# Performance work log

Hardware: AMD Instinct MI355X
Metric: run time of the kernel (lower is better)

## Reference

```python
import jax, jax.numpy as jnp
import numpy as np
import math

NUM_CLASS = 100000
EMB = 512
N = 1024
S = 64.0
M2 = 0.5
M3 = 0.2
T = 0.2
ERRSUM = 0.3
CLEAR_RIO = 1.0 - ERRSUM
NUM_ALL = 2900.0
GAMMA = 2
EMA = 0.01


def setup_inputs() -> dict:
    key = jax.random.key(0)
    k1, k2, k3 = jax.random.split(key, 3)
    logits = jax.random.normal(k1, (N, EMB), dtype=jnp.float32)
    labels = jax.random.randint(k2, (N,), 0, NUM_CLASS, dtype=jnp.int64)
    weight = jax.random.normal(k3, (NUM_CLASS, EMB), dtype=jnp.float32) * 0.01
    return {"logits": logits, "labels": labels, "weight": weight}


def _l2norm(x):
    return x * jax.lax.rsqrt(jnp.sum(x * x, axis=-1, keepdims=True) + 1e-12)


def reference(logits, labels, weight):
    # margin constants (m_smooth starts at 0, so margin_ada leaves m3 unchanged)
    cos_m, sin_m = math.cos(M2), math.sin(M2)
    theta = math.cos(math.pi - M2)
    sinmm = math.sin(math.pi - M2) * M2
    cos_m_, sin_m_ = math.cos(M3), math.sin(M3)
    sinmm_ = math.sin(-M3) * M3

    # cosine similarity GEMM: [N, C]
    cos = jnp.clip(_l2norm(logits) @ _l2norm(weight).T, -1.0, 1.0)

    rows = jnp.arange(cos.shape[0])
    tgt = cos[rows, labels]                       # [N]
    sin_theta = jnp.sqrt(1.0 - tgt * tgt)
    cos_theta_m = tgt * cos_m - sin_theta * sin_m
    cos_theta_m_ = tgt * cos_m_ - sin_theta * sin_m_
    ftl = jnp.where(tgt > theta, cos_theta_m, tgt - sinmm)          # hard margin
    ftl_ = jnp.where(tgt <= cos_m_, cos_theta_m_, tgt + sinmm_)     # noise margin

    mask_hard = cos > ftl[:, None]
    mask_noise = cos > ftl_[:, None]

    # m_smooth update (pure counting -> non-differentiable constant)
    hard_cnt = jnp.sum(mask_hard).astype(jnp.float32)
    m_smooth = ((NUM_ALL - hard_cnt) / NUM_ALL) * EMA  # prev m_smooth = 0
    noise_scale = (1.0 - m_smooth / CLEAR_RIO) ** GAMMA

    out = jnp.where(mask_hard, cos * (T + 1.0), cos)
    out = jnp.where(mask_noise, jnp.maximum(cos * noise_scale, 1e-30), out)
    out = out.at[rows, labels].set(ftl)
    return out * S
```

## Files before the change

### kernel.cpp

```cpp
#include <hip/hip_runtime.h>
#include <hip/hip_bf16.h>
#include <stdint.h>

#define NUM_CLASS 100000
#define CPAD      100096
#define EMB       512
#define NROW      1024

#define BM 128
#define BN 128
#define BK 64
#define LROW 72

typedef __bf16 bf16x8 __attribute__((ext_vector_type(8)));
typedef float  f32x4  __attribute__((ext_vector_type(4)));

#define WS_FTL  256
#define WS_FTL2 4352
#define WS_A    8704
#define WS_B    1057280

__device__ inline unsigned short f2bf(float x) {
    uint32_t u = __builtin_bit_cast(uint32_t, x);
    uint32_t r = u + 0x7FFFu + ((u >> 16) & 1u);
    return (unsigned short)(r >> 16);
}
__device__ inline unsigned int pack2(float a, float b) {
    return (unsigned int)f2bf(a) | ((unsigned int)f2bf(b) << 16);
}

__global__ __launch_bounds__(256) void prep_a(const float* __restrict__ logits,
                                              unsigned short* __restrict__ A) {
    int wave = threadIdx.x >> 6, lane = threadIdx.x & 63;
    int row = blockIdx.x * 4 + wave;
    const float4* src = (const float4*)(logits + (size_t)row * EMB + lane * 8);
    float4 a = src[0], b = src[1];
    float ss = a.x*a.x + a.y*a.y + a.z*a.z + a.w*a.w
             + b.x*b.x + b.y*b.y + b.z*b.z + b.w*b.w;
    for (int off = 32; off; off >>= 1) ss += __shfl_xor(ss, off, 64);
    float rs = rsqrtf(ss + 1e-12f);
    uint4 o;
    o.x = pack2(a.x*rs, a.y*rs); o.y = pack2(a.z*rs, a.w*rs);
    o.z = pack2(b.x*rs, b.y*rs); o.w = pack2(b.z*rs, b.w*rs);
    *(uint4*)(A + (size_t)row * EMB + lane * 8) = o;
}

__global__ __launch_bounds__(256) void prep_b(const float* __restrict__ w,
                                              unsigned short* __restrict__ B) {
    int wave = threadIdx.x >> 6, lane = threadIdx.x & 63;
    int row = blockIdx.x * 4 + wave;
    uint4 o = {0u, 0u, 0u, 0u};
    if (row < NUM_CLASS) {
        const float4* src = (const float4*)(w + (size_t)row * EMB + lane * 8);
        float4 a = src[0], b = src[1];
        float ss = a.x*a.x + a.y*a.y + a.z*a.z + a.w*a.w
                 + b.x*b.x + b.y*b.y + b.z*b.z + b.w*b.w;
        for (int off = 32; off; off >>= 1) ss += __shfl_xor(ss, off, 64);
        float rs = rsqrtf(ss + 1e-12f);
        o.x = pack2(a.x*rs, a.y*rs); o.y = pack2(a.z*rs, a.w*rs);
        o.z = pack2(b.x*rs, b.y*rs); o.w = pack2(b.z*rs, b.w*rs);
    }
    *(uint4*)(B + (size_t)row * EMB + lane * 8) = o;
}

__global__ __launch_bounds__(64) void prep_rows(const float* __restrict__ logits,
                                                const float* __restrict__ w,
                                                const int* __restrict__ labels,
                                                float* __restrict__ ftl,
                                                float* __restrict__ ftl2,
                                                unsigned int* __restrict__ cnt) {
    int row = blockIdx.x, lane = threadIdx.x;
    if (row == 0 && lane == 0) *cnt = 0u;
    int lab = labels[row];
    const float4* lp = (const float4*)(logits + (size_t)row * EMB + lane * 8);
    const float4* wp = (const float4*)(w + (size_t)lab * EMB + lane * 8);
    float4 l0 = lp[0], l1 = lp[1], w0 = wp[0], w1 = wp[1];
    float sl = l0.x*l0.x + l0.y*l0.y + l0.z*l0.z + l0.w*l0.w
             + l1.x*l1.x + l1.y*l1.y + l1.z*l1.z + l1.w*l1.w;
    float sw = w0.x*w0.x + w0.y*w0.y + w0.z*w0.z + w0.w*w0.w
             + w1.x*w1.x + w1.y*w1.y + w1.z*w1.z + w1.w*w1.w;
    float d  = l0.x*w0.x + l0.y*w0.y + l0.z*w0.z + l0.w*w0.w
             + l1.x*w1.x + l1.y*w1.y + l1.z*w1.z + l1.w*w1.w;
    for (int off = 32; off; off >>= 1) {
        sl += __shfl_xor(sl, off, 64);
        sw += __shfl_xor(sw, off, 64);
        d  += __shfl_xor(d,  off, 64);
    }
    if (lane == 0) {
        float tgt = d * rsqrtf(sl + 1e-12f) * rsqrtf(sw + 1e-12f);
        tgt = fminf(1.0f, fmaxf(-1.0f, tgt));
        const float cos_m  = 0.8775825618903728f;
        const float sin_m  = 0.479425538604203f;
        const float theta  = -0.8775825618903728f;
        const float sinmm  = 0.2397127693021015f;
        const float cos_m_ = 0.9800665778412416f;
        const float sin_m_ = 0.19866933079506122f;
        const float sinmm_ = -0.03973386615901225f;
        float st   = sqrtf(fmaxf(0.0f, 1.0f - tgt * tgt));
        float ctm  = tgt * cos_m  - st * sin_m;
        float ctm_ = tgt * cos_m_ - st * sin_m_;
        ftl[row]  = (tgt > theta)    ? ctm  : (tgt - sinmm);
        ftl2[row] = (tgt <= cos_m_)  ? ctm_ : (tgt + sinmm_);
    }
}

__global__ __launch_bounds__(256) void gemm_count(const unsigned short* __restrict__ A,
                                                  const unsigned short* __restrict__ B,
                                                  const float* __restrict__ ftl,
                                                  float* __restrict__ out,
                                                  unsigned int* __restrict__ cnt) {
    __shared__ __align__(16) unsigned short lA[BM * LROW];
    __shared__ __align__(16) unsigned short lB[BN * LROW];
    int tid = threadIdx.x;
    int wave = tid >> 6, lane = tid & 63;
    int wm = wave >> 1, wn = wave & 1;
    int quad = lane >> 4, l16 = lane & 15;
    int bn = blockIdx.x, bm = blockIdx.y;

    f32x4 acc[4][4] = {};

    int srow  = tid >> 3;
    int sslot = tid & 7;
    const size_t a_base = ((size_t)bm * BM + srow) * EMB + sslot * 8;
    const size_t b_base = ((size_t)bn * BN + srow) * EMB + sslot * 8;

    for (int kk = 0; kk < EMB / BK; ++kk) {
        __syncthreads();
        int k0 = kk * BK;
#pragma unroll
        for (int r = 0; r < 4; ++r) {
            uint4 va = *(const uint4*)(A + a_base + (size_t)r * 32 * EMB + k0);
            uint4 vb = *(const uint4*)(B + b_base + (size_t)r * 32 * EMB + k0);
            *(uint4*)&lA[(srow + r * 32) * LROW + sslot * 8] = va;
            *(uint4*)&lB[(srow + r * 32) * LROW + sslot * 8] = vb;
        }
        __syncthreads();
#pragma unroll
        for (int ks = 0; ks < 2; ++ks) {
            bf16x8 af[4], bfr[4];
#pragma unroll
            for (int i = 0; i < 4; ++i) {
                int ar = wm * 64 + i * 16 + l16;
                af[i]  = *(const bf16x8*)&lA[ar * LROW + ks * 32 + quad * 8];
                int br = wn * 64 + i * 16 + l16;
                bfr[i] = *(const bf16x8*)&lB[br * LROW + ks * 32 + quad * 8];
            }
#pragma unroll
            for (int i = 0; i < 4; ++i)
#pragma unroll
                for (int j = 0; j < 4; ++j)
                    acc[i][j] = __builtin_amdgcn_mfma_f32_16x16x32_bf16(af[i], bfr[j], acc[i][j], 0, 0, 0);
        }
    }

    int local = 0;
#pragma unroll
    for (int i = 0; i < 4; ++i) {
        int row0 = bm * BM + wm * 64 + i * 16 + quad * 4;
        float f0 = ftl[row0], f1 = ftl[row0 + 1], f2 = ftl[row0 + 2], f3 = ftl[row0 + 3];
#pragma unroll
        for (int j = 0; j < 4; ++j) {
            int col = bn * BN + wn * 64 + j * 16 + l16;
            bool cv = col < NUM_CLASS;
#pragma unroll
            for (int r = 0; r < 4; ++r) {
                float c = acc[i][j][r];
                c = fminf(1.0f, fmaxf(-1.0f, c));
                if (cv) {
                    float fr = (r == 0) ? f0 : (r == 1) ? f1 : (r == 2) ? f2 : f3;
                    local += (c > fr) ? 1 : 0;
                    out[(size_t)(row0 + r) * NUM_CLASS + col] = c;
                }
            }
        }
    }
    for (int off = 32; off; off >>= 1) local += __shfl_down(local, off, 64);
    if (lane == 0) atomicAdd(cnt, (unsigned int)local);
}

__global__ __launch_bounds__(256) void apply_k(float* __restrict__ out,
                                               const float* __restrict__ ftl,
                                               const float* __restrict__ ftl2,
                                               const int* __restrict__ labels,
                                               const unsigned int* __restrict__ cnt) {
    int row = blockIdx.y;
    int c4 = blockIdx.x * blockDim.x + threadIdx.x;
    if (c4 >= NUM_CLASS / 4) return;
    float h = (float)(*cnt);
    float msm = ((2900.0f - h) / 2900.0f) * 0.01f;
    float t = 1.0f - msm / 0.7f;
    float ns = t * t;
    float f = ftl[row], f2 = ftl2[row];
    int lab = labels[row];
    float4* p = (float4*)(out + (size_t)row * NUM_CLASS) + c4;
    float4 v = *p;
    float r[4] = {v.x, v.y, v.z, v.w};
    int col = c4 * 4;
#pragma unroll
    for (int q = 0; q < 4; ++q) {
        float c = r[q];
        float o = (c > f) ? c * 1.2f : c;
        if (c > f2) o = fmaxf(c * ns, 1e-30f);
        if (col + q == lab) o = f;
        r[q] = o * 64.0f;
    }
    *p = make_float4(r[0], r[1], r[2], r[3]);
}

extern "C" void kernel_launch(void* const* d_in, const int* in_sizes, int n_in,
                              void* d_out, int out_size, void* d_ws, size_t ws_size,
                              hipStream_t stream) {
    const float* logits = (const float*)d_in[0];
    const int*   labels = (const int*)d_in[1];
    const float* weight = (const float*)d_in[2];
    char* ws = (char*)d_ws;
    unsigned int*  cnt  = (unsigned int*)ws;
    float*         ftl  = (float*)(ws + WS_FTL);
    float*         ftl2 = (float*)(ws + WS_FTL2);
    unsigned short* A   = (unsigned short*)(ws + WS_A);
    unsigned short* B   = (unsigned short*)(ws + WS_B);
    float* out = (float*)d_out;

    prep_a<<<NROW / 4, 256, 0, stream>>>(logits, A);
    prep_b<<<CPAD / 4, 256, 0, stream>>>(weight, B);
    prep_rows<<<NROW, 64, 0, stream>>>(logits, weight, labels, ftl, ftl2, cnt);
    gemm_count<<<dim3(CPAD / BN, NROW / BM), 256, 0, stream>>>(A, B, ftl, out, cnt);
    apply_k<<<dim3((NUM_CLASS / 4 + 255) / 256, NROW), 256, 0, stream>>>(out, ftl, ftl2, labels, cnt);
}
```

Before: 1.004 ms.

## Use direct global-to-LDS loads in GEMM, swap grid order, flatten apply grid

The GEMM tile staging now uses global_load_lds to copy 16-byte chunks straight into an unpadded LDS layout, skipping the register round-trip. The barrier is moved to the end of the k loop. The grid is transposed so that consecutive blocks share the same B column tile across the 8 row tiles, which improves L2 reuse of the weight matrix. The apply kernel now uses a flat 1D grid that covers exactly 1024×25000 float4s, with no bounds check and no idle threads. In exchange, the unpadded LDS rows (64 bf16 stride) can cause bank conflicts on the fragment reads.

New measurement: 976.5 us. 1.03x faster.

```diff
diff --git a/kernel.cpp b/kernel.cpp
--- a/kernel.cpp
+++ b/kernel.cpp
@@ -10,7 +10,6 @@
 #define BM 128
 #define BN 128
 #define BK 64
-#define LROW 72
 
 typedef __bf16 bf16x8 __attribute__((ext_vector_type(8)));
 typedef float  f32x4  __attribute__((ext_vector_type(4)));
@@ -27,6 +26,13 @@
 }
 __device__ inline unsigned int pack2(float a, float b) {
     return (unsigned int)f2bf(a) | ((unsigned int)f2bf(b) << 16);
+}
+
+__device__ __forceinline__ void gld16(const unsigned short* g, unsigned short* l) {
+    __builtin_amdgcn_global_load_lds(
+        (const __attribute__((address_space(1))) unsigned int*)g,
+        (__attribute__((address_space(3))) unsigned int*)l,
+        16, 0, 0);
 }
 
 __global__ __launch_bounds__(256) void prep_a(const float* __restrict__ logits,
@@ -109,30 +115,30 @@
                                                   const float* __restrict__ ftl,
                                                   float* __restrict__ out,
                                                   unsigned int* __restrict__ cnt) {
-    __shared__ __align__(16) unsigned short lA[BM * LROW];
-    __shared__ __align__(16) unsigned short lB[BN * LROW];
+    __shared__ __align__(16) unsigned short lA[BM * BK];
+    __shared__ __align__(16) unsigned short lB[BN * BK];
     int tid = threadIdx.x;
     int wave = tid >> 6, lane = tid & 63;
     int wm = wave >> 1, wn = wave & 1;
     int quad = lane >> 4, l16 = lane & 15;
-    int bn = blockIdx.x, bm = blockIdx.y;
+    int bm = blockIdx.x, bn = blockIdx.y;
 
     f32x4 acc[4][4] = {};
 
     int srow  = tid >> 3;
     int sslot = tid & 7;
-    const size_t a_base = ((size_t)bm * BM + srow) * EMB + sslot * 8;
-    const size_t b_base = ((size_t)bn * BN + srow) * EMB + sslot * 8;
-
+    const unsigned short* a_src = A + ((size_t)bm * BM + srow) * EMB + sslot * 8;
+    const unsigned short* b_src = B + ((size_t)bn * BN + srow) * EMB + sslot * 8;
+    unsigned short* a_dst = &lA[tid * 8];
+    unsigned short* b_dst = &lB[tid * 8];
+
+#pragma unroll 1
     for (int kk = 0; kk < EMB / BK; ++kk) {
-        __syncthreads();
         int k0 = kk * BK;
 #pragma unroll
         for (int r = 0; r < 4; ++r) {
-            uint4 va = *(const uint4*)(A + a_base + (size_t)r * 32 * EMB + k0);
-            uint4 vb = *(const uint4*)(B + b_base + (size_t)r * 32 * EMB + k0);
-            *(uint4*)&lA[(srow + r * 32) * LROW + sslot * 8] = va;
-            *(uint4*)&lB[(srow + r * 32) * LROW + sslot * 8] = vb;
+            gld16(a_src + (size_t)r * 32 * EMB + k0, a_dst + r * 32 * BK);
+            gld16(b_src + (size_t)r * 32 * EMB + k0, b_dst + r * 32 * BK);
         }
         __syncthreads();
 #pragma unroll
@@ -141,9 +147,9 @@
 #pragma unroll
             for (int i = 0; i < 4; ++i) {
                 int ar = wm * 64 + i * 16 + l16;
-                af[i]  = *(const bf16x8*)&lA[ar * LROW + ks * 32 + quad * 8];
+                af[i]  = *(const bf16x8*)&lA[ar * BK + ks * 32 + quad * 8];
                 int br = wn * 64 + i * 16 + l16;
-                bfr[i] = *(const bf16x8*)&lB[br * LROW + ks * 32 + quad * 8];
+                bfr[i] = *(const bf16x8*)&lB[br * BK + ks * 32 + quad * 8];
             }
 #pragma unroll
             for (int i = 0; i < 4; ++i)
@@ -151,6 +157,7 @@
                 for (int j = 0; j < 4; ++j)
                     acc[i][j] = __builtin_amdgcn_mfma_f32_16x16x32_bf16(af[i], bfr[j], acc[i][j], 0, 0, 0);
         }
+        __syncthreads();
     }
 
     int local = 0;
@@ -183,9 +190,9 @@
                                                const float* __restrict__ ftl2,
                                                const int* __restrict__ labels,
                                                const unsigned int* __restrict__ cnt) {
-    int row = blockIdx.y;
-    int c4 = blockIdx.x * blockDim.x + threadIdx.x;
-    if (c4 >= NUM_CLASS / 4) return;
+    int idx = blockIdx.x * 256 + threadIdx.x;
+    int row = idx / 25000;
+    int c4  = idx - row * 25000;
     float h = (float)(*cnt);
     float msm = ((2900.0f - h) / 2900.0f) * 0.01f;
     float t = 1.0f - msm / 0.7f;
@@ -224,6 +231,6 @@
     prep_a<<<NROW / 4, 256, 0, stream>>>(logits, A);
     prep_b<<<CPAD / 4, 256, 0, stream>>>(weight, B);
     prep_rows<<<NROW, 64, 0, stream>>>(logits, weight, labels, ftl, ftl2, cnt);
-    gemm_count<<<dim3(CPAD / BN, NROW / BM), 256, 0, stream>>>(A, B, ftl, out, cnt);
-    apply_k<<<dim3((NUM_CLASS / 4 + 255) / 256, NROW), 256, 0, stream>>>(out, ftl, ftl2, labels, cnt);
-}
+    gemm_count<<<dim3(NROW / BM, CPAD / BN), 256, 0, stream>>>(A, B, ftl, out, cnt);
+    apply_k<<<100000, 256, 0, stream>>>(out, ftl, ftl2, labels, cnt);
+}
```
